# Optimization experiments

Measured on AMD Instinct MI355X. Metric: run time of the kernel, lower is better.

The kernel has to match this reference:

```python
import jax, jax.numpy as jnp
import numpy as np

K = 9   # kernel_size (neighbors)
D = 1   # dilation


def setup_inputs() -> dict:
    key = jax.random.key(0)
    k1, k2 = jax.random.split(key)
    B, C, N, OUT = 8, 64, 4096, 128
    x = jax.random.normal(k1, (B, C, N), dtype=jnp.float32)
    W = jax.random.normal(k2, (OUT, 2 * C), dtype=jnp.float32) * 0.05
    b = jnp.zeros((OUT,), dtype=jnp.float32)
    return {"x": x, "W": W, "b": b}


def dilated_knn(x, k, d):
    # x: [B, C, N] -> nn_idx: [B, N, k] (indices of k nearest neighbors, dilated)
    x = jax.lax.stop_gradient(x)  # original detaches x for graph construction
    x2 = jnp.sum(x * x, axis=1)                      # [B, N]
    inner = jnp.einsum('bcn,bcm->bnm', x, x)         # [B, N, N]
    neg_dist = 2.0 * inner - x2[:, :, None] - x2[:, None, :]  # -||xi-xj||^2
    _, idx = jax.lax.top_k(neg_dist, k * d)          # [B, N, k*d]
    return idx[..., ::d]                             # dilated selection -> [B, N, k]


def reference(x, W, b):
    # x: [B, C, N]
    nn_idx = dilated_knn(x, K, D)                    # [B, N, k]
    # gather neighbor features: x_j[b, c, n, kk] = x[b, c, nn_idx[b, n, kk]]
    x_j = jax.vmap(lambda xb, ib: xb[:, ib])(x, nn_idx)  # [B, C, N, k]
    # max-relative: max_k (x_j - x_i)
    x_max = jnp.max(x_j - x[:, :, :, None], axis=-1)     # [B, C, N]
    h = jnp.concatenate([x, x_max], axis=1)              # [B, 2C, N]
    # 1x1 conv + bias + ReLU
    out = jnp.einsum('oc,bcn->bon', W, h) + b[None, :, None]
    return jax.nn.relu(out)
```

## Files before the change

### kernel.cpp

```cpp
#include <hip/hip_runtime.h>
#include <float.h>

#define B_   8
#define C_   64
#define N_   4096
#define OUT_ 128
#define KNN  9
#define CAP  64
#define TAU_A 2.15f

typedef __attribute__((ext_vector_type(8))) short short8;
typedef __attribute__((ext_vector_type(4))) float f32x4;

__device__ inline unsigned short f2bf(float f) {
    unsigned u = __float_as_uint(f);
    unsigned r = (u + 0x7fffu + ((u >> 16) & 1u)) >> 16;
    return (unsigned short)r;
}
__device__ inline float bf2f(unsigned short s) {
    return __uint_as_float(((unsigned)s) << 16);
}


__global__ void k_wt(const float* __restrict__ W, unsigned short* __restrict__ wfrag) {
    int mt = blockIdx.x, kc = threadIdx.x >> 6, L = threadIdx.x & 63;
    int o  = mt * 16 + (L & 15);
    int c0 = kc * 32 + ((L >> 4) * 8);
    const float* src = W + (size_t)o * 128 + c0;
    float4 v0 = *(const float4*)src, v1 = *(const float4*)(src + 4);
    float vs[8] = {v0.x, v0.y, v0.z, v0.w, v1.x, v1.y, v1.z, v1.w};
    short8 hi, lo;
#pragma unroll
    for (int j = 0; j < 8; ++j) {
        unsigned short hb = f2bf(vs[j]);
        float hf = bf2f(hb);
        lo[j] = (short)f2bf(vs[j] - hf);
        hi[j] = (short)hb;
    }
    size_t cb = (size_t)(mt * 4 + kc) * 2 * 512;
    *(short8*)(wfrag + cb + L * 8)       = hi;
    *(short8*)(wfrag + cb + 512 + L * 8) = lo;
}

__global__ void k_transpose(const float* __restrict__ x, float* __restrict__ xT,
                            float* __restrict__ x2, unsigned short* __restrict__ xfrag) {
    __shared__ float t[C_][65];
    int b  = blockIdx.x & 7;
    int n0 = (blockIdx.x >> 3) * 64;
    int tid = threadIdx.x;
    for (int i = 0; i < 16; ++i) {
        int e = i * 256 + tid;
        int c = e >> 6, nn = e & 63;
        t[c][nn] = x[((size_t)b * C_ + c) * N_ + n0 + nn];
    }
    __syncthreads();
    for (int i = 0; i < 16; ++i) {
        int e = i * 256 + tid;
        int nn = e >> 6, c = e & 63;
        xT[((size_t)b * N_ + n0 + nn) * C_ + c] = t[c][nn];
    }
    int q = tid >> 6, L = tid & 63;
    int mloc = q * 16 + (L & 15);
    int k8 = (L >> 4) * 8;
    size_t cb = (size_t)(b * 256 + (n0 >> 4) + q) * 2 * 512;
#pragma unroll
    for (int h = 0; h < 2; ++h) {
        short8 hi;
#pragma unroll
        for (int j = 0; j < 8; ++j)
            hi[j] = (short)f2bf(t[h * 32 + k8 + j][mloc]);
        *(short8*)(xfrag + cb + h * 512 + L * 8) = hi;
    }
    if (tid < 64) {
        float s = 0.f;
        for (int c = 0; c < C_; ++c) { float v = t[c][tid]; s += v * v; }
        x2[(size_t)b * N_ + n0 + tid] = s;
    }
}

#define APPEND(KEY, TAU, LN, MIDX)                                      \
    if ((KEY) > (TAU)) {                                                \
        unsigned u = __float_as_uint(KEY);                              \
        u = (u & 0x80000000u) ? ~u : (u | 0x80000000u);                 \
        unsigned pk = (u & 0xFFFFF000u) | (unsigned)(MIDX);             \
        int sl = atomicAdd(&cnt_s[LN], 1);                              \
        if (sl < CAP) buf_s[LN][sl] = pk;                               \
    }

__global__ __launch_bounds__(512, 4) void k_topk_mf(const unsigned short* __restrict__ xfrag,
                                                    const float* __restrict__ x2,
                                                    unsigned* __restrict__ cand24,
                                                    int* __restrict__ cnt2) {
    __shared__ int cnt_s[64];
    __shared__ unsigned buf_s[64][CAP];
    int b    = blockIdx.x & 7;
    int mh   = (blockIdx.x >> 3) & 1;
    int ng   = blockIdx.x >> 4;
    int wave = threadIdx.x >> 6, lane = threadIdx.x & 63;
    if (threadIdx.x < 64) cnt_s[threadIdx.x] = 0;

    const short8* fr = (const short8*)xfrag;

    short8 Bh[4][2];
#pragma unroll
    for (int q = 0; q < 4; ++q)
#pragma unroll
        for (int h = 0; h < 2; ++h) {
            int ch = ((b * 256 + ng * 4 + q) * 2 + h);
            Bh[q][h] = fr[(size_t)ch * 64 + lane];
        }

    float tau[4];
#pragma unroll
    for (int q = 0; q < 4; ++q) {
        float x2n = x2[b * N_ + ng * 64 + q * 16 + (lane & 15)];
        tau[q] = TAU_A * sqrtf(fmaf(4.f, x2n, 128.f)) - 64.f;
    }

    int mt0 = mh * 128 + wave * 16;
    const short8* pA = fr + (size_t)(b * 256 + mt0) * 2 * 64 + lane;
    const f32x4*  px2 = (const f32x4*)(x2 + b * N_ + mt0 * 16 + (lane >> 4) * 4);
    short8 Ah0 = pA[0], Ah1 = pA[64];
    f32x4 x2v = *px2;

    __syncthreads();

    for (int i = 0; i < 16; ++i) {
        if (i != 15) { pA += 128; px2 += 4; }
        short8 nAh0 = pA[0], nAh1 = pA[64];
        f32x4 nx2 = *px2;

        int mbase = (mt0 + i) * 16 + (lane >> 4) * 4;

#pragma unroll
        for (int q = 0; q < 4; ++q) {
            f32x4 acc = {0.f, 0.f, 0.f, 0.f};
            acc = __builtin_amdgcn_mfma_f32_16x16x32_bf16(Ah0, Bh[q][0], acc, 0, 0, 0);
            acc = __builtin_amdgcn_mfma_f32_16x16x32_bf16(Ah1, Bh[q][1], acc, 0, 0, 0);
            float k0 = fmaf(2.f, acc[0], -x2v[0]);
            float k1 = fmaf(2.f, acc[1], -x2v[1]);
            float k2 = fmaf(2.f, acc[2], -x2v[2]);
            float k3 = fmaf(2.f, acc[3], -x2v[3]);
            float kmax = fmaxf(fmaxf(k0, k1), fmaxf(k2, k3));
            if (kmax > tau[q]) {
                int ln = q * 16 + (lane & 15);
                APPEND(k0, tau[q], ln, mbase + 0)
                APPEND(k1, tau[q], ln, mbase + 1)
                APPEND(k2, tau[q], ln, mbase + 2)
                APPEND(k3, tau[q], ln, mbase + 3)
            }
        }
        Ah0 = nAh0; Ah1 = nAh1; x2v = nx2;
    }

    __syncthreads();
    if (threadIdx.x < 64) {
        int r = threadIdx.x;
        int c = cnt_s[r];
        size_t grow = (size_t)b * N_ + ng * 64 + r;
        cnt2[grow * 2 + mh] = c;
        int cc = min(c, CAP);
        unsigned best[12];
#pragma unroll
        for (int j = 0; j < 12; ++j) best[j] = 0u;
        for (int s = 0; s < cc; ++s) {
            unsigned v = buf_s[r][s];
            if (v > best[0]) {
                best[0] = v;
#pragma unroll
                for (int j = 0; j < 11; ++j) {
                    bool sw = best[j] > best[j + 1];
                    unsigned t = best[j];
                    best[j]     = sw ? best[j + 1] : best[j];
                    best[j + 1] = sw ? t : best[j + 1];
                }
            }
        }
#pragma unroll
        for (int j = 0; j < 12; ++j)
            cand24[grow * 24 + mh * 12 + j] = best[11 - j];
    }
}

__global__ __launch_bounds__(256) void k_refine(const float* __restrict__ xT,
                                                const unsigned* __restrict__ cand24,
                                                const int* __restrict__ cnt2,
                                                int* __restrict__ idx9) {
    __shared__ double kk[4][2][24];
    __shared__ int    ki[4][2][24];
    int wave = threadIdx.x >> 6, lane = threadIdx.x & 63;
    int half = lane >> 5, hl = lane & 31;
    int b = blockIdx.x & 7;
    int row = b * N_ + (blockIdx.x >> 3) * 8 + wave * 2 + half;
    int c0 = cnt2[(size_t)row * 2 + 0];
    int c1 = cnt2[(size_t)row * 2 + 1];
    bool ok = (c0 + c1 >= KNN) && (c0 <= CAP) && (c1 <= CAP);
    int c0c = min(c0, 12), c1c = min(c1, 12);

    double mykey = -1e300; int myidx = 0x7fffffff;
    bool valid = ok && (hl < 24) && ((hl < 12) ? (hl < c0c) : ((hl - 12) < c1c));
    if (valid) {
        int m = (int)(cand24[(size_t)row * 24 + hl] & 0xFFFu);
        const float* xi = xT + (size_t)row * C_;
        const float* xm = xT + (((size_t)b << 12) + m) * C_;
        double d0 = 0.0, d1 = 0.0, s0 = 0.0, s1 = 0.0;
#pragma unroll
        for (int c4 = 0; c4 < 16; c4 += 2) {
            float4 a0 = *(const float4*)(xi + c4 * 4);
            float4 a1 = *(const float4*)(xi + c4 * 4 + 4);
            float4 v0 = *(const float4*)(xm + c4 * 4);
            float4 v1 = *(const float4*)(xm + c4 * 4 + 4);
            d0 = fma((double)a0.x, (double)v0.x, d0);  s0 = fma((double)v0.x, (double)v0.x, s0);
            d0 = fma((double)a0.y, (double)v0.y, d0);  s0 = fma((double)v0.y, (double)v0.y, s0);
            d0 = fma((double)a0.z, (double)v0.z, d0);  s0 = fma((double)v0.z, (double)v0.z, s0);
            d0 = fma((double)a0.w, (double)v0.w, d0);  s0 = fma((double)v0.w, (double)v0.w, s0);
            d1 = fma((double)a1.x, (double)v1.x, d1);  s1 = fma((double)v1.x, (double)v1.x, s1);
            d1 = fma((double)a1.y, (double)v1.y, d1);  s1 = fma((double)v1.y, (double)v1.y, s1);
            d1 = fma((double)a1.z, (double)v1.z, d1);  s1 = fma((double)v1.z, (double)v1.z, s1);
            d1 = fma((double)a1.w, (double)v1.w, d1);  s1 = fma((double)v1.w, (double)v1.w, s1);
        }
        mykey = 2.0 * (d0 + d1) - (s0 + s1);
        myidx = m;
    }
    if (hl < 24) { kk[wave][half][hl] = mykey; ki[wave][half][hl] = myidx; }
    if (valid) {
        int r = 0;
#pragma unroll
        for (int k = 0; k < 24; ++k) {
            double ok2 = kk[wave][half][k]; int oi = ki[wave][half][k];
            r += (ok2 > mykey || (ok2 == mykey && oi < myidx)) ? 1 : 0;
        }
        if (r < KNN) idx9[(size_t)row * KNN + r] = myidx;
    }
}

__global__ void k_fallback(const float* __restrict__ xT, const int* __restrict__ cnt2,
                           int* __restrict__ idx9) {
    int wave = threadIdx.x >> 6, lane = threadIdx.x & 63;
    int row = blockIdx.x * 4 + wave;
    int c0 = cnt2[(size_t)row * 2 + 0];
    int c1 = cnt2[(size_t)row * 2 + 1];
    if ((c0 + c1 >= KNN) && (c0 <= CAP) && (c1 <= CAP)) return;
    int b = row >> 12;
    const float* xi = xT + (size_t)row * C_;
    float4 xr[16];
#pragma unroll
    for (int c4 = 0; c4 < 16; ++c4) xr[c4] = *(const float4*)(xi + c4 * 4);
    double sk[9]; int si[9];
#pragma unroll
    for (int j = 0; j < 9; ++j) { sk[j] = -1e300; si[j] = 0x7fffffff; }
    for (int mb = 0; mb < N_; mb += 64) {
        int m = mb + lane;
        const float* xm = xT + (((size_t)b << 12) + m) * C_;
        double d0 = 0.0, d1 = 0.0, s0 = 0.0, s1 = 0.0;
#pragma unroll
        for (int c4 = 0; c4 < 16; c4 += 2) {
            float4 v = *(const float4*)(xm + c4 * 4);
            float4 w = *(const float4*)(xm + c4 * 4 + 4);
            float4 a = xr[c4], bb = xr[c4 + 1];
            d0 = fma((double)a.x, (double)v.x, d0);  s0 = fma((double)v.x, (double)v.x, s0);
            d0 = fma((double)a.y, (double)v.y, d0);  s0 = fma((double)v.y, (double)v.y, s0);
            d0 = fma((double)a.z, (double)v.z, d0);  s0 = fma((double)v.z, (double)v.z, s0);
            d0 = fma((double)a.w, (double)v.w, d0);  s0 = fma((double)v.w, (double)v.w, s0);
            d1 = fma((double)bb.x, (double)w.x, d1); s1 = fma((double)w.x, (double)w.x, s1);
            d1 = fma((double)bb.y, (double)w.y, d1); s1 = fma((double)w.y, (double)w.y, s1);
            d1 = fma((double)bb.z, (double)w.z, d1); s1 = fma((double)w.z, (double)w.z, s1);
            d1 = fma((double)bb.w, (double)w.w, d1); s1 = fma((double)w.w, (double)w.w, s1);
        }
        double key = 2.0 * (d0 + d1) - (s0 + s1);
        if (key > sk[0] || (key == sk[0] && m < si[0])) {
            sk[0] = key; si[0] = m;
#pragma unroll
            for (int j = 0; j < 8; ++j) {
                bool sw = (sk[j] > sk[j + 1]) || (sk[j] == sk[j + 1] && si[j] < si[j + 1]);
                double tk = sk[j]; int ti = si[j];
                sk[j]     = sw ? sk[j + 1] : sk[j];
                si[j]     = sw ? si[j + 1] : si[j];
                sk[j + 1] = sw ? tk : sk[j + 1];
                si[j + 1] = sw ? ti : si[j + 1];
            }
        }
    }
    for (int r = 0; r < KNN; ++r) {
        double k = sk[8]; int ix = si[8];
#pragma unroll
        for (int o = 32; o; o >>= 1) {
            double ok = __shfl_xor(k, o); int oi = __shfl_xor(ix, o);
            bool take = (ok > k) || (ok == k && oi < ix);
            k = take ? ok : k; ix = take ? oi : ix;
        }
        if (lane == 0) idx9[(size_t)row * KNN + r] = ix;
        if (si[8] == ix) {
#pragma unroll
            for (int j = 8; j > 0; --j) { sk[j] = sk[j - 1]; si[j] = si[j - 1]; }
            sk[0] = -1e300; si[0] = 0x7fffffff;
        }
    }
}

__global__ __launch_bounds__(256, 2) void k_gemm(const float* __restrict__ xT,
                                                 const int* __restrict__ idx9,
                                                 const unsigned short* __restrict__ wfrag,
                                                 const float* __restrict__ bias,
                                                 float* __restrict__ out) {
    __shared__ float h[128][65];
    int b  = blockIdx.x & 7;
    int n0 = (blockIdx.x >> 3) * 64;
    int wave = threadIdx.x >> 6, lane = threadIdx.x & 63;

    const short8* fw = (const short8*)wfrag;
    short8 Wh[2][4], Wl[2][4];
#pragma unroll
    for (int t = 0; t < 2; ++t)
#pragma unroll
        for (int kc = 0; kc < 4; ++kc) {
            size_t cb = (size_t)((wave * 2 + t) * 4 + kc) * 2 * 64;
            Wh[t][kc] = fw[cb + lane];
            Wl[t][kc] = fw[cb + 64 + lane];
        }

    for (int r = 0; r < 16; ++r) {
        int nn = wave * 16 + r;
        size_t row = (size_t)b * N_ + n0 + nn;
        const int* id = idx9 + row * KNN;
        float m = -FLT_MAX;
#pragma unroll
        for (int k = 0; k < KNN; ++k) {
            int j = id[k];
            m = fmaxf(m, xT[(((size_t)b << 12) + j) * C_ + lane]);
        }
        float xic = xT[row * C_ + lane];
        h[lane][nn]      = xic;
        h[64 + lane][nn] = m - xic;
    }
    __syncthreads();

    f32x4 acc[2][4];
#pragma unroll
    for (int t = 0; t < 2; ++t)
#pragma unroll
        for (int nt = 0; nt < 4; ++nt) acc[t][nt] = (f32x4){0.f, 0.f, 0.f, 0.f};

    int cb0 = (lane >> 4) * 8;
    int nl  = lane & 15;
#pragma unroll
    for (int kc = 0; kc < 4; ++kc) {
#pragma unroll
        for (int nt = 0; nt < 4; ++nt) {
            short8 bh, bl;
#pragma unroll
            for (int j = 0; j < 8; ++j) {
                float v = h[kc * 32 + cb0 + j][nt * 16 + nl];
                unsigned short hb = f2bf(v);
                bl[j] = (short)f2bf(v - bf2f(hb));
                bh[j] = (short)hb;
            }
#pragma unroll
            for (int t = 0; t < 2; ++t) {
                acc[t][nt] = __builtin_amdgcn_mfma_f32_16x16x32_bf16(Wh[t][kc], bh, acc[t][nt], 0, 0, 0);
                acc[t][nt] = __builtin_amdgcn_mfma_f32_16x16x32_bf16(Wl[t][kc], bh, acc[t][nt], 0, 0, 0);
                acc[t][nt] = __builtin_amdgcn_mfma_f32_16x16x32_bf16(Wh[t][kc], bl, acc[t][nt], 0, 0, 0);
            }
        }
    }
    __syncthreads();

    f32x4 bs[2];
#pragma unroll
    for (int t = 0; t < 2; ++t)
        bs[t] = *(const f32x4*)(bias + wave * 32 + t * 16 + (lane >> 4) * 4);
#pragma unroll
    for (int t = 0; t < 2; ++t)
#pragma unroll
        for (int nt = 0; nt < 4; ++nt)
#pragma unroll
            for (int j = 0; j < 4; ++j) {
                float v = acc[t][nt][j] + bs[t][j];
                h[wave * 32 + t * 16 + (lane >> 4) * 4 + j][nt * 16 + nl] = fmaxf(v, 0.f);
            }
    __syncthreads();

#pragma unroll
    for (int rr = 0; rr < 32; ++rr) {
        int o = wave * 32 + rr;
        out[((size_t)b * OUT_ + o) * N_ + n0 + lane] = h[o][lane];
    }
}

extern "C" void kernel_launch(void* const* d_in, const int* in_sizes, int n_in,
                              void* d_out, int out_size, void* d_ws, size_t ws_size,
                              hipStream_t stream) {
    const float* x    = (const float*)d_in[0];
    const float* W    = (const float*)d_in[1];
    const float* bias = (const float*)d_in[2];
    float* out = (float*)d_out;
    char* ws = (char*)d_ws;

    float*          xT     = (float*)(ws);
    unsigned short* xfrag  = (unsigned short*)(ws + 8388608);
    int*            idx9   = (int*)(ws + 8388608);
    float*          x2     = (float*)(ws + 16777216);
    unsigned short* wfrag  = (unsigned short*)(ws + 16908288);
    unsigned*       cand24 = (unsigned*)(ws + 16973824);
    int*            cnt2   = (int*)(ws + 20119552);

    k_wt       <<<dim3(8),    dim3(256), 0, stream>>>(W, wfrag);
    k_transpose<<<dim3(512),  dim3(256), 0, stream>>>(x, xT, x2, xfrag);
    k_topk_mf  <<<dim3(1024), dim3(512), 0, stream>>>(xfrag, x2, cand24, cnt2);
    k_refine   <<<dim3(4096), dim3(256), 0, stream>>>(xT, cand24, cnt2, idx9);
    k_fallback <<<dim3(8192), dim3(256), 0, stream>>>(xT, cnt2, idx9);
    k_gemm     <<<dim3(512),  dim3(256), 0, stream>>>(xT, idx9, wfrag, bias, out);
}
```

Before: 116.9 us.

## Fold weight prep into transpose, fallback scan into refine, vectorize transpose

Merges the weight-fragment conversion into extra blocks of the transpose kernel and moves the full-scan fallback into the refine kernel as a per-row device function, which removes two kernel launches. The transpose now uses float4 loads and stores instead of scalar accesses. Fallback rows are handled inline by the refine wave, so a rare slow row can stall its block, and the fallback no longer caches the query row in registers.

```diff
diff --git a/kernel.cpp b/kernel.cpp
--- a/kernel.cpp
+++ b/kernel.cpp
@@ -22,42 +22,50 @@
 }
 
 
-__global__ void k_wt(const float* __restrict__ W, unsigned short* __restrict__ wfrag) {
-    int mt = blockIdx.x, kc = threadIdx.x >> 6, L = threadIdx.x & 63;
-    int o  = mt * 16 + (L & 15);
-    int c0 = kc * 32 + ((L >> 4) * 8);
-    const float* src = W + (size_t)o * 128 + c0;
-    float4 v0 = *(const float4*)src, v1 = *(const float4*)(src + 4);
-    float vs[8] = {v0.x, v0.y, v0.z, v0.w, v1.x, v1.y, v1.z, v1.w};
-    short8 hi, lo;
-#pragma unroll
-    for (int j = 0; j < 8; ++j) {
-        unsigned short hb = f2bf(vs[j]);
-        float hf = bf2f(hb);
-        lo[j] = (short)f2bf(vs[j] - hf);
-        hi[j] = (short)hb;
-    }
-    size_t cb = (size_t)(mt * 4 + kc) * 2 * 512;
-    *(short8*)(wfrag + cb + L * 8)       = hi;
-    *(short8*)(wfrag + cb + 512 + L * 8) = lo;
-}
-
 __global__ void k_transpose(const float* __restrict__ x, float* __restrict__ xT,
-                            float* __restrict__ x2, unsigned short* __restrict__ xfrag) {
+                            float* __restrict__ x2, unsigned short* __restrict__ xfrag,
+                            const float* __restrict__ W, unsigned short* __restrict__ wfrag) {
     __shared__ float t[C_][65];
+    int tid = threadIdx.x;
+    if (blockIdx.x >= 512) {
+        int mt = blockIdx.x - 512;
+        int kc = tid >> 6, L = tid & 63;
+        int o  = mt * 16 + (L & 15);
+        int c0 = kc * 32 + ((L >> 4) * 8);
+        const float* src = W + (size_t)o * 128 + c0;
+        float4 v0 = *(const float4*)src, v1 = *(const float4*)(src + 4);
+        float vs[8] = {v0.x, v0.y, v0.z, v0.w, v1.x, v1.y, v1.z, v1.w};
+        short8 hi, lo;
+#pragma unroll
+        for (int j = 0; j < 8; ++j) {
+            unsigned short hb = f2bf(vs[j]);
+            float hf = bf2f(hb);
+            lo[j] = (short)f2bf(vs[j] - hf);
+            hi[j] = (short)hb;
+        }
+        size_t cb = (size_t)(mt * 4 + kc) * 2 * 512;
+        *(short8*)(wfrag + cb + L * 8)       = hi;
+        *(short8*)(wfrag + cb + 512 + L * 8) = lo;
+        return;
+    }
     int b  = blockIdx.x & 7;
     int n0 = (blockIdx.x >> 3) * 64;
-    int tid = threadIdx.x;
-    for (int i = 0; i < 16; ++i) {
-        int e = i * 256 + tid;
-        int c = e >> 6, nn = e & 63;
-        t[c][nn] = x[((size_t)b * C_ + c) * N_ + n0 + nn];
-    }
-    __syncthreads();
-    for (int i = 0; i < 16; ++i) {
-        int e = i * 256 + tid;
-        int nn = e >> 6, c = e & 63;
-        xT[((size_t)b * N_ + n0 + nn) * C_ + c] = t[c][nn];
+    for (int i = 0; i < 4; ++i) {
+        int f = i * 256 + tid;
+        int c = f >> 4, n4 = f & 15;
+        float4 v = *(const float4*)(x + ((size_t)b * C_ + c) * N_ + n0 + n4 * 4);
+        t[c][n4 * 4 + 0] = v.x;
+        t[c][n4 * 4 + 1] = v.y;
+        t[c][n4 * 4 + 2] = v.z;
+        t[c][n4 * 4 + 3] = v.w;
+    }
+    __syncthreads();
+    for (int i = 0; i < 4; ++i) {
+        int f = i * 256 + tid;
+        int n = f >> 4, c4 = f & 15;
+        float4 v = {t[c4 * 4 + 0][n], t[c4 * 4 + 1][n],
+                    t[c4 * 4 + 2][n], t[c4 * 4 + 3][n]};
+        *(float4*)(xT + ((size_t)b * N_ + n0 + n) * C_ + c4 * 4) = v;
     }
     int q = tid >> 6, L = tid & 63;
     int mloc = q * 16 + (L & 15);
@@ -182,6 +190,62 @@
     }
 }
 
+__device__ void fullscan_row(const float* __restrict__ xT, int b, int row, int lane,
+                             int* __restrict__ idx9) {
+    const float* xi = xT + (size_t)row * C_;
+    double sk[9]; int si[9];
+#pragma unroll
+    for (int j = 0; j < 9; ++j) { sk[j] = -1e300; si[j] = 0x7fffffff; }
+    for (int mb = 0; mb < N_; mb += 64) {
+        int m = mb + lane;
+        const float* xm = xT + (((size_t)b << 12) + m) * C_;
+        double d0 = 0.0, d1 = 0.0, s0 = 0.0, s1 = 0.0;
+#pragma unroll
+        for (int c4 = 0; c4 < 16; c4 += 2) {
+            float4 a = *(const float4*)(xi + c4 * 4);
+            float4 bb = *(const float4*)(xi + c4 * 4 + 4);
+            float4 v = *(const float4*)(xm + c4 * 4);
+            float4 w = *(const float4*)(xm + c4 * 4 + 4);
+            d0 = fma((double)a.x, (double)v.x, d0);  s0 = fma((double)v.x, (double)v.x, s0);
+            d0 = fma((double)a.y, (double)v.y, d0);  s0 = fma((double)v.y, (double)v.y, s0);
+            d0 = fma((double)a.z, (double)v.z, d0);  s0 = fma((double)v.z, (double)v.z, s0);
+            d0 = fma((double)a.w, (double)v.w, d0);  s0 = fma((double)v.w, (double)v.w, s0);
+            d1 = fma((double)bb.x, (double)w.x, d1); s1 = fma((double)w.x, (double)w.x, s1);
+            d1 = fma((double)bb.y, (double)w.y, d1); s1 = fma((double)w.y, (double)w.y, s1);
+            d1 = fma((double)bb.z, (double)w.z, d1); s1 = fma((double)w.z, (double)w.z, s1);
+            d1 = fma((double)bb.w, (double)w.w, d1); s1 = fma((double)w.w, (double)w.w, s1);
+        }
+        double key = 2.0 * (d0 + d1) - (s0 + s1);
+        if (key > sk[0] || (key == sk[0] && m < si[0])) {
+            sk[0] = key; si[0] = m;
+#pragma unroll
+            for (int j = 0; j < 8; ++j) {
+                bool sw = (sk[j] > sk[j + 1]) || (sk[j] == sk[j + 1] && si[j] < si[j + 1]);
+                double tk = sk[j]; int ti = si[j];
+                sk[j]     = sw ? sk[j + 1] : sk[j];
+                si[j]     = sw ? si[j + 1] : si[j];
+                sk[j + 1] = sw ? tk : sk[j + 1];
+                si[j + 1] = sw ? ti : si[j + 1];
+            }
+        }
+    }
+    for (int r = 0; r < KNN; ++r) {
+        double k = sk[8]; int ix = si[8];
+#pragma unroll
+        for (int o = 32; o; o >>= 1) {
+            double ok = __shfl_xor(k, o); int oi = __shfl_xor(ix, o);
+            bool take = (ok > k) || (ok == k && oi < ix);
+            k = take ? ok : k; ix = take ? oi : ix;
+        }
+        if (lane == 0) idx9[(size_t)row * KNN + r] = ix;
+        if (si[8] == ix) {
+#pragma unroll
+            for (int j = 8; j > 0; --j) { sk[j] = sk[j - 1]; si[j] = si[j - 1]; }
+            sk[0] = -1e300; si[0] = 0x7fffffff;
+        }
+    }
+}
+
 __global__ __launch_bounds__(256) void k_refine(const float* __restrict__ xT,
                                                 const unsigned* __restrict__ cand24,
                                                 const int* __restrict__ cnt2,
@@ -191,10 +255,14 @@
     int wave = threadIdx.x >> 6, lane = threadIdx.x & 63;
     int half = lane >> 5, hl = lane & 31;
     int b = blockIdx.x & 7;
-    int row = b * N_ + (blockIdx.x >> 3) * 8 + wave * 2 + half;
-    int c0 = cnt2[(size_t)row * 2 + 0];
-    int c1 = cnt2[(size_t)row * 2 + 1];
-    bool ok = (c0 + c1 >= KNN) && (c0 <= CAP) && (c1 <= CAP);
+    int rowbase = b * N_ + (blockIdx.x >> 3) * 8 + wave * 2;
+    int row = rowbase + half;
+    int c00 = cnt2[(size_t)rowbase * 2 + 0], c01 = cnt2[(size_t)rowbase * 2 + 1];
+    int c10 = cnt2[(size_t)(rowbase + 1) * 2 + 0], c11 = cnt2[(size_t)(rowbase + 1) * 2 + 1];
+    bool ok0 = (c00 + c01 >= KNN) && (c00 <= CAP) && (c01 <= CAP);
+    bool ok1 = (c10 + c11 >= KNN) && (c10 <= CAP) && (c11 <= CAP);
+    bool ok = half ? ok1 : ok0;
+    int c0 = half ? c10 : c00, c1 = half ? c11 : c01;
     int c0c = min(c0, 12), c1c = min(c1, 12);
 
     double mykey = -1e300; int myidx = 0x7fffffff;
@@ -232,70 +300,8 @@
         }
         if (r < KNN) idx9[(size_t)row * KNN + r] = myidx;
     }
-}
-
-__global__ void k_fallback(const float* __restrict__ xT, const int* __restrict__ cnt2,
-                           int* __restrict__ idx9) {
-    int wave = threadIdx.x >> 6, lane = threadIdx.x & 63;
-    int row = blockIdx.x * 4 + wave;
-    int c0 = cnt2[(size_t)row * 2 + 0];
-    int c1 = cnt2[(size_t)row * 2 + 1];
-    if ((c0 + c1 >= KNN) && (c0 <= CAP) && (c1 <= CAP)) return;
-    int b = row >> 12;
-    const float* xi = xT + (size_t)row * C_;
-    float4 xr[16];
-#pragma unroll
-    for (int c4 = 0; c4 < 16; ++c4) xr[c4] = *(const float4*)(xi + c4 * 4);
-    double sk[9]; int si[9];
-#pragma unroll
-    for (int j = 0; j < 9; ++j) { sk[j] = -1e300; si[j] = 0x7fffffff; }
-    for (int mb = 0; mb < N_; mb += 64) {
-        int m = mb + lane;
-        const float* xm = xT + (((size_t)b << 12) + m) * C_;
-        double d0 = 0.0, d1 = 0.0, s0 = 0.0, s1 = 0.0;
-#pragma unroll
-        for (int c4 = 0; c4 < 16; c4 += 2) {
-            float4 v = *(const float4*)(xm + c4 * 4);
-            float4 w = *(const float4*)(xm + c4 * 4 + 4);
-            float4 a = xr[c4], bb = xr[c4 + 1];
-            d0 = fma((double)a.x, (double)v.x, d0);  s0 = fma((double)v.x, (double)v.x, s0);
-            d0 = fma((double)a.y, (double)v.y, d0);  s0 = fma((double)v.y, (double)v.y, s0);
-            d0 = fma((double)a.z, (double)v.z, d0);  s0 = fma((double)v.z, (double)v.z, s0);
-            d0 = fma((double)a.w, (double)v.w, d0);  s0 = fma((double)v.w, (double)v.w, s0);
-            d1 = fma((double)bb.x, (double)w.x, d1); s1 = fma((double)w.x, (double)w.x, s1);
-            d1 = fma((double)bb.y, (double)w.y, d1); s1 = fma((double)w.y, (double)w.y, s1);
-            d1 = fma((double)bb.z, (double)w.z, d1); s1 = fma((double)w.z, (double)w.z, s1);
-            d1 = fma((double)bb.w, (double)w.w, d1); s1 = fma((double)w.w, (double)w.w, s1);
-        }
-        double key = 2.0 * (d0 + d1) - (s0 + s1);
-        if (key > sk[0] || (key == sk[0] && m < si[0])) {
-            sk[0] = key; si[0] = m;
-#pragma unroll
-            for (int j = 0; j < 8; ++j) {
-                bool sw = (sk[j] > sk[j + 1]) || (sk[j] == sk[j + 1] && si[j] < si[j + 1]);
-                double tk = sk[j]; int ti = si[j];
-                sk[j]     = sw ? sk[j + 1] : sk[j];
-                si[j]     = sw ? si[j + 1] : si[j];
-                sk[j + 1] = sw ? tk : sk[j + 1];
-                si[j + 1] = sw ? ti : si[j + 1];
-            }
-        }
-    }
-    for (int r = 0; r < KNN; ++r) {
-        double k = sk[8]; int ix = si[8];
-#pragma unroll
-        for (int o = 32; o; o >>= 1) {
-            double ok = __shfl_xor(k, o); int oi = __shfl_xor(ix, o);
-            bool take = (ok > k) || (ok == k && oi < ix);
-            k = take ? ok : k; ix = take ? oi : ix;
-        }
-        if (lane == 0) idx9[(size_t)row * KNN + r] = ix;
-        if (si[8] == ix) {
-#pragma unroll
-            for (int j = 8; j > 0; --j) { sk[j] = sk[j - 1]; si[j] = si[j - 1]; }
-            sk[0] = -1e300; si[0] = 0x7fffffff;
-        }
-    }
+    if (!ok0) fullscan_row(xT, b, rowbase, lane, idx9);
+    if (!ok1) fullscan_row(xT, b, rowbase + 1, lane, idx9);
 }
 
 __global__ __launch_bounds__(256, 2) void k_gemm(const float* __restrict__ xT,
@@ -404,10 +410,8 @@
     unsigned*       cand24 = (unsigned*)(ws + 16973824);
     int*            cnt2   = (int*)(ws + 20119552);
 
-    k_wt       <<<dim3(8),    dim3(256), 0, stream>>>(W, wfrag);
-    k_transpose<<<dim3(512),  dim3(256), 0, stream>>>(x, xT, x2, xfrag);
+    k_transpose<<<dim3(520),  dim3(256), 0, stream>>>(x, xT, x2, xfrag, W, wfrag);
     k_topk_mf  <<<dim3(1024), dim3(512), 0, stream>>>(xfrag, x2, cand24, cnt2);
     k_refine   <<<dim3(4096), dim3(256), 0, stream>>>(xT, cand24, cnt2, idx9);
-    k_fallback <<<dim3(8192), dim3(256), 0, stream>>>(xT, cnt2, idx9);
     k_gemm     <<<dim3(512),  dim3(256), 0, stream>>>(xT, idx9, wfrag, bias, out);
 }
```

Result: slower. 146.8 us (+25.5%).
